# Performance work log

Measured on AMD Instinct MI355X. Metric: run time of the kernel, lower is better.

The kernel has to match this reference:

```python
import jax, jax.numpy as jnp
import numpy as np

N = 4096
F_IN = 256
F_OUT = 64
H = 4
ALPHA = 0.2  # leaky_relu negative slope
NEG_BIG = -9e15


def setup_inputs() -> dict:
    key = jax.random.key(0)
    k1, k2, k3, k4 = jax.random.split(key, 4)
    x = jax.random.normal(k1, (N, F_IN), dtype=jnp.float32)
    adj = jax.random.randint(k2, (N, N), 0, 2, dtype=jnp.int32)
    # xavier-uniform-like init for params
    limW = float(np.sqrt(6.0 / (F_IN + F_OUT)))
    W = jax.random.uniform(k3, (H, F_IN, F_OUT), jnp.float32, -limW, limW)
    lima = float(np.sqrt(6.0 / (2 * F_OUT + 1)))
    a = jax.random.uniform(k4, (H, 2 * F_OUT, 1), jnp.float32, -lima, lima)
    return {"x": x, "adj": adj, "W": W, "a": a}


def reference(x, adj, W, a):
    # Wh[h,n,o] = x @ W[h]
    Wh = jnp.einsum('nf,hfo->hno', x, W)
    # split attention vector: e[h,i,j] = leaky_relu(a1.Wh_i + a2.Wh_j)
    a1 = a[:, :F_OUT, 0]   # [H, F_OUT]
    a2 = a[:, F_OUT:, 0]   # [H, F_OUT]
    s1 = jnp.einsum('hno,ho->hn', Wh, a1)  # [H, N]
    s2 = jnp.einsum('hno,ho->hn', Wh, a2)  # [H, N]
    e = jax.nn.leaky_relu(s1[:, :, None] + s2[:, None, :], ALPHA)  # [H, N, N]
    e = jnp.where(adj[None, :, :] > 0, e, NEG_BIG)
    att = jax.nn.softmax(e, axis=-1)
    # dropout=0 (eval-mode reference)
    h_prime = jnp.einsum('hij,hjo->hio', att, Wh)  # [H, N, F_OUT]
    # concat heads -> [N, H*F_OUT]
    return jnp.transpose(h_prime, (1, 0, 2)).reshape(N, H * F_OUT)
```

## Files before the change

kernel.cpp:

```cpp
#include <hip/hip_runtime.h>

#define NN 4096
#define FIN 256
#define FOUT 64
#define NH 4

using f32x4 = __attribute__((ext_vector_type(4))) float;
using s16x8 = __attribute__((ext_vector_type(8))) short;
typedef unsigned long long u64;

__device__ __forceinline__ unsigned short f32_to_bf16_rne(float f) {
    unsigned b = __float_as_uint(f);
    b += 0x7FFFu + ((b >> 16) & 1u);
    return (unsigned short)(b >> 16);
}

__global__ __launch_bounds__(256) void k_prep(
    const float* __restrict__ x, const float* __restrict__ W,
    const float* __restrict__ a, const int* __restrict__ adj,
    short* __restrict__ WhT, float* __restrict__ s1, float* __restrict__ s2,
    float* __restrict__ blockmax, u64* __restrict__ packed)
{
    __shared__ unsigned short xs[64 * 256];
    __shared__ unsigned short wt[64 * 256];
    __shared__ float s2red[16];
    const int bx = blockIdx.x;
    const int t = threadIdx.x;

    if (bx >= 256) {
        const int lane = t & 63;
        const int jc = t >> 6;
        const int row = bx - 256;
        const int g = lane >> 4;
        const int li = lane & 15;
        const int* ap = adj + (size_t)row * NN + jc * 1024 + lane * 4;
        int4 v0 = *(const int4*)(ap);
        int4 v1 = *(const int4*)(ap + 256);
        int4 v2 = *(const int4*)(ap + 512);
        int4 v3 = *(const int4*)(ap + 768);
        u64 words[4];
        int4 vv[4] = {v0, v1, v2, v3};
        #pragma unroll
        for (int k = 0; k < 4; ++k) {
            unsigned b = (vv[k].x != 0 ? 1u : 0u) | (vv[k].y != 0 ? 2u : 0u)
                       | (vv[k].z != 0 ? 4u : 0u) | (vv[k].w != 0 ? 8u : 0u);
            u64 field = (u64)b << (4 * li);
            field |= __shfl_xor(field, 1, 64);
            field |= __shfl_xor(field, 2, 64);
            field |= __shfl_xor(field, 4, 64);
            field |= __shfl_xor(field, 8, 64);
            words[k] = field;
        }
        if (li == 0) {
            #pragma unroll
            for (int k = 0; k < 4; ++k)
                packed[(size_t)(jc * 16 + 4 * k + g) * NN + row] = words[k];
        }
        return;
    }

    const int nb = bx & 63, h = bx >> 6;
    const int n0 = nb * 64;
    {
        const float4* xg = reinterpret_cast<const float4*>(x + (size_t)n0 * FIN);
        for (int k = t; k < 64 * FIN / 4; k += 256) {
            float4 v = xg[k];
            int row = k >> 6, fq = k & 63;
            u64 pk = (u64)f32_to_bf16_rne(v.x) | ((u64)f32_to_bf16_rne(v.y) << 16)
                   | ((u64)f32_to_bf16_rne(v.z) << 32) | ((u64)f32_to_bf16_rne(v.w) << 48);
            int byte = (row * 512 + fq * 8) ^ ((row & 7) << 4);
            *(u64*)((char*)xs + byte) = pk;
        }
        const float* Wg = W + (size_t)h * FIN * FOUT;
        for (int k = t; k < FIN * FOUT; k += 256) {
            int f = k >> 6, o = k & 63;
            unsigned short wv = f32_to_bf16_rne(Wg[k]);
            int byte = (o * 512 + f * 2) ^ ((o & 7) << 4);
            *(unsigned short*)((char*)wt + byte) = wv;
        }
    }
    __syncthreads();
    const int lane = t & 63, wv_ = t >> 6;
    const int rowA = lane & 15;
    const int kq = (lane >> 4) * 8;
    const int i0 = wv_ * 16;
    f32x4 acc[4];
    #pragma unroll
    for (int c = 0; c < 4; ++c) acc[c] = (f32x4){0.f, 0.f, 0.f, 0.f};
    const int arow = i0 + rowA;
    #pragma unroll
    for (int kb = 0; kb < FIN; kb += 32) {
        int ab = (arow * 512 + (kb + kq) * 2) ^ ((arow & 7) << 4);
        s16x8 af = *(const s16x8*)((char*)xs + ab);
        #pragma unroll
        for (int c = 0; c < 4; ++c) {
            int col = c * 16 + rowA;
            int bb = (col * 512 + (kb + kq) * 2) ^ ((col & 7) << 4);
            s16x8 bf = *(const s16x8*)((char*)wt + bb);
            acc[c] = __builtin_amdgcn_mfma_f32_16x16x32_bf16(af, bf, acc[c], 0, 0, 0);
        }
    }
    const int q0 = (lane >> 4) * 4;
    const float L2E = 1.4426950408889634f;
    float v1acc[4] = {0.f, 0.f, 0.f, 0.f}, v2acc[4] = {0.f, 0.f, 0.f, 0.f};
    #pragma unroll
    for (int c = 0; c < 4; ++c) {
        int col = c * 16 + rowA;
        float a1v = a[h * (2 * FOUT) + col];
        float a2v = a[h * (2 * FOUT) + FOUT + col];
        short* wp = WhT + ((size_t)(h * FOUT + col)) * NN + n0 + i0 + q0;
        alignas(8) unsigned short tmp[4];
        #pragma unroll
        for (int q = 0; q < 4; ++q) {
            float v = acc[c][q];
            tmp[q] = f32_to_bf16_rne(v);
            v1acc[q] = fmaf(v, a1v, v1acc[q]);
            v2acc[q] = fmaf(v, a2v, v2acc[q]);
        }
        __builtin_memcpy(wp, tmp, 8);
    }
    float wmax = -3.0e38f;
    #pragma unroll
    for (int q = 0; q < 4; ++q) {
        float v1 = v1acc[q] * L2E, v2 = v2acc[q] * L2E;
        #pragma unroll
        for (int d = 1; d < 16; d <<= 1) {
            v1 += __shfl_xor(v1, d, 64);
            v2 += __shfl_xor(v2, d, 64);
        }
        if (rowA == 0) {
            int n = n0 + i0 + q0 + q;
            s1[h * NN + n] = v1;
            s2[h * NN + n] = v2;
            wmax = fmaxf(wmax, v2);
        }
    }
    if (rowA == 0) s2red[wv_ * 4 + (lane >> 4)] = wmax;
    __syncthreads();
    if (t == 0) {
        float m = s2red[0];
        #pragma unroll
        for (int i = 1; i < 16; ++i) m = fmaxf(m, s2red[i]);
        blockmax[h * 64 + nb] = m;
    }
}

__global__ __launch_bounds__(1024, 4) void k_attn(
    const u64* __restrict__ packed, const short* __restrict__ WhT,
    const float* __restrict__ s1, const float* __restrict__ blockmax,
    const float* __restrict__ s2, float* __restrict__ out)
{
    __shared__ __align__(16) char smraw[16 * 1040 * 4];
    const int t = threadIdx.x;
    const int lane = t & 63;
    const int wid = t >> 6;
    const int rg = wid >> 2;
    const int jq = wid & 3;
    const int ib64 = blockIdx.x;
    const int h = blockIdx.y;
    const int row16 = lane & 15;
    const int kbase = (lane >> 4) * 8;
    const int irow = ib64 * 64 + rg * 16 + row16;

    float bm = blockmax[h * 64 + lane];
    #pragma unroll
    for (int d = 32; d >= 1; d >>= 1) bm = fmaxf(bm, __shfl_xor(bm, d, 64));
    const float s1v = s1[h * NN + irow];
    const float ttv = s1v + bm;
    const float M = fmaxf(ttv, 0.2f * ttv);
    const float c1v = s1v - M;
    const float c2v = fmaf(0.2f, s1v, -M);

    f32x4 acc[4], acc_l;
    #pragma unroll
    for (int c = 0; c < 4; ++c) acc[c] = (f32x4){0.f, 0.f, 0.f, 0.f};
    acc_l = (f32x4){0.f, 0.f, 0.f, 0.f};
    s16x8 ones;
    #pragma unroll
    for (int i = 0; i < 8; ++i) ones[i] = (short)0x3F80;

    const float* s2q = s2 + h * NN + kbase;
    const u64*   mb  = packed + irow;

    const int gt = rg * 64 + lane;
    const int so = gt >> 3;
    const int sj = (gt & 7) * 8;
    const short* wsrc = WhT + (size_t)h * FOUT * NN;
    char* btb = smraw + jq * 16384;
    const int wb0 = (so * 128 + sj * 2) ^ ((so & 7) << 4);
    const int wb1 = ((so + 32) * 128 + sj * 2) ^ ((so & 7) << 4);

    int rd[4][2];
    #pragma unroll
    for (int c = 0; c < 4; ++c) {
        int o = c * 16 + row16;
        #pragma unroll
        for (int hf = 0; hf < 2; ++hf)
            rd[c][hf] = (o * 128 + (hf * 32 + kbase) * 2) ^ ((o & 7) << 4);
    }

    auto mk = [&](float sa, float sb, unsigned bits, int q0) -> unsigned {
        float e0 = fmaxf(c1v + sa, fmaf(0.2f, sa, c2v));
        float e1 = fmaxf(c1v + sb, fmaf(0.2f, sb, c2v));
        float p0 = __builtin_amdgcn_exp2f(e0);
        float p1 = __builtin_amdgcn_exp2f(e1);
        p0 = (bits & (1u << q0)) ? p0 : 0.f;
        p1 = (bits & (2u << q0)) ? p1 : 0.f;
        unsigned pk;
        asm("v_cvt_pk_bf16_f32 %0, %1, %2" : "=v"(pk) : "v"(p0), "v"(p1));
        return pk;
    };

    const int jbase = jq * 1024;
    auto body = [&](int jb, char* btr, char* btw, u64 cm, f32x4 (&cs)[4],
                    u64& nm, f32x4 (&ns)[4]) {
        int jn = jb + 64;
        int jpf = (jn < jbase + 1024) ? jn : jbase;
        s16x8 st0 = *(const s16x8*)(wsrc + (size_t)so * NN + jpf + sj);
        s16x8 st1 = *(const s16x8*)(wsrc + (size_t)(so + 32) * NN + jpf + sj);
        nm = mb[(size_t)(jpf >> 6) * NN];
        ns[0] = *(const f32x4*)(s2q + jpf);
        ns[1] = *(const f32x4*)(s2q + jpf + 4);
        ns[2] = *(const f32x4*)(s2q + jpf + 32);
        ns[3] = *(const f32x4*)(s2q + jpf + 36);
        unsigned ml8 = ((unsigned)cm >> kbase) & 0xFFu;
        unsigned mh8 = ((unsigned)(cm >> 32) >> kbase) & 0xFFu;
        s16x8 A0, A1;
        unsigned* A0u = reinterpret_cast<unsigned*>(&A0);
        unsigned* A1u = reinterpret_cast<unsigned*>(&A1);
        A0u[0] = mk(cs[0][0], cs[0][1], ml8, 0);
        A0u[1] = mk(cs[0][2], cs[0][3], ml8, 2);
        A0u[2] = mk(cs[1][0], cs[1][1], ml8, 4);
        A0u[3] = mk(cs[1][2], cs[1][3], ml8, 6);
        A1u[0] = mk(cs[2][0], cs[2][1], mh8, 0);
        A1u[1] = mk(cs[2][2], cs[2][3], mh8, 2);
        A1u[2] = mk(cs[3][0], cs[3][1], mh8, 4);
        A1u[3] = mk(cs[3][2], cs[3][3], mh8, 6);
        *(s16x8*)(btw + wb0) = st0;
        *(s16x8*)(btw + wb1) = st1;
        s16x8 b00 = *(const s16x8*)(btr + rd[0][0]);
        s16x8 b01 = *(const s16x8*)(btr + rd[0][1]);
        s16x8 b10 = *(const s16x8*)(btr + rd[1][0]);
        s16x8 b11 = *(const s16x8*)(btr + rd[1][1]);
        s16x8 b20 = *(const s16x8*)(btr + rd[2][0]);
        s16x8 b21 = *(const s16x8*)(btr + rd[2][1]);
        s16x8 b30 = *(const s16x8*)(btr + rd[3][0]);
        s16x8 b31 = *(const s16x8*)(btr + rd[3][1]);
        acc_l  = __builtin_amdgcn_mfma_f32_16x16x32_bf16(A0, ones, acc_l, 0, 0, 0);
        acc_l  = __builtin_amdgcn_mfma_f32_16x16x32_bf16(A1, ones, acc_l, 0, 0, 0);
        acc[0] = __builtin_amdgcn_mfma_f32_16x16x32_bf16(A0, b00, acc[0], 0, 0, 0);
        acc[0] = __builtin_amdgcn_mfma_f32_16x16x32_bf16(A1, b01, acc[0], 0, 0, 0);
        acc[1] = __builtin_amdgcn_mfma_f32_16x16x32_bf16(A0, b10, acc[1], 0, 0, 0);
        acc[1] = __builtin_amdgcn_mfma_f32_16x16x32_bf16(A1, b11, acc[1], 0, 0, 0);
        acc[2] = __builtin_amdgcn_mfma_f32_16x16x32_bf16(A0, b20, acc[2], 0, 0, 0);
        acc[2] = __builtin_amdgcn_mfma_f32_16x16x32_bf16(A1, b21, acc[2], 0, 0, 0);
        acc[3] = __builtin_amdgcn_mfma_f32_16x16x32_bf16(A0, b30, acc[3], 0, 0, 0);
        acc[3] = __builtin_amdgcn_mfma_f32_16x16x32_bf16(A1, b31, acc[3], 0, 0, 0);
    };

    u64 m0, m1;
    f32x4 sv0[4], sv1[4];
    int jb = jbase;
    {
        s16x8 st0 = *(const s16x8*)(wsrc + (size_t)so * NN + jb + sj);
        s16x8 st1 = *(const s16x8*)(wsrc + (size_t)(so + 32) * NN + jb + sj);
        *(s16x8*)(btb + wb0) = st0;
        *(s16x8*)(btb + wb1) = st1;
        m0 = mb[(size_t)(jb >> 6) * NN];
        sv0[0] = *(const f32x4*)(s2q + jb);
        sv0[1] = *(const f32x4*)(s2q + jb + 4);
        sv0[2] = *(const f32x4*)(s2q + jb + 32);
        sv0[3] = *(const f32x4*)(s2q + jb + 36);
    }
    __syncthreads();
    #pragma unroll 1
    for (int it = 0; it < 8; ++it) {
        body(jb, btb, btb + 8192, m0, sv0, m1, sv1);
        __syncthreads();
        body(jb + 64, btb + 8192, btb, m1, sv1, m0, sv0);
        __syncthreads();
        jb += 128;
    }

    float* mw = (float*)smraw + wid * 1040;
    #pragma unroll
    for (int c = 0; c < 4; ++c) {
        #pragma unroll
        for (int q = 0; q < 4; ++q) {
            int r = (lane >> 4) * 4 + q;
            int o = c * 16 + row16;
            mw[r * 64 + o] = acc[c][q];
        }
    }
    if (row16 == 0) {
        #pragma unroll
        for (int q = 0; q < 4; ++q) mw[1024 + (lane >> 4) * 4 + q] = acc_l[q];
    }
    __syncthreads();
    if (jq == 0) {
        const float* p0 = (float*)smraw + (rg * 4 + 0) * 1040;
        const float* p1 = (float*)smraw + (rg * 4 + 1) * 1040;
        const float* p2 = (float*)smraw + (rg * 4 + 2) * 1040;
        const float* p3 = (float*)smraw + (rg * 4 + 3) * 1040;
        #pragma unroll
        for (int k = 0; k < 16; ++k) {
            int idx = k * 64 + lane;
            int r = idx >> 6;
            float v = p0[idx] + p1[idx] + p2[idx] + p3[idx];
            float l = p0[1024 + r] + p1[1024 + r] + p2[1024 + r] + p3[1024 + r];
            int n = ib64 * 64 + rg * 16 + r;
            out[(size_t)n * (NH * FOUT) + h * FOUT + (idx & 63)] = v / l;
        }
    }
}

extern "C" void kernel_launch(void* const* d_in, const int* in_sizes, int n_in,
                              void* d_out, int out_size, void* d_ws, size_t ws_size,
                              hipStream_t stream) {
    (void)in_sizes; (void)n_in; (void)out_size; (void)ws_size;
    const float* x  = (const float*)d_in[0];
    const int*  adj = (const int*)d_in[1];
    const float* W  = (const float*)d_in[2];
    const float* a  = (const float*)d_in[3];
    float* out = (float*)d_out;
    char* ws = (char*)d_ws;

    size_t off = 0;
    short* WhT      = (short*)(ws + off); off += (size_t)NH * FOUT * NN * 2;
    float* s1       = (float*)(ws + off); off += (size_t)NH * NN * 4;
    float* s2       = (float*)(ws + off); off += (size_t)NH * NN * 4;
    float* blockmax = (float*)(ws + off); off += (size_t)NH * 64 * 4;
    u64* packed     = (u64*)(ws + off); off += (size_t)(NN / 64) * NN * 8;

    k_prep<<<4352, 256, 0, stream>>>(x, W, a, adj, WhT, s1, s2, blockmax, packed);
    k_attn<<<dim3(64, NH), 1024, 0, stream>>>(packed, WhT, s1, blockmax, s2, out);
}
```

Baseline: 52.95 us.

## Split attention key range across two blocks and merge partials in new kernel

The attention kernel grid gains a z dimension of 2, and each block now covers half of the key columns, so there are 512 blocks instead of 256 on the device. Each block writes its unnormalized partial accumulators and row sums to a workspace buffer. A new merge kernel adds the two partials and divides by the summed normalizer. The aim is better CU occupancy (256 blocks underfill the MI355X), at the cost of an extra launch and a partial-buffer round trip through global memory.

```diff
diff --git a/kernel.cpp b/kernel.cpp
--- a/kernel.cpp
+++ b/kernel.cpp
@@ -148,7 +148,7 @@
 __global__ __launch_bounds__(1024, 4) void k_attn(
     const u64* __restrict__ packed, const short* __restrict__ WhT,
     const float* __restrict__ s1, const float* __restrict__ blockmax,
-    const float* __restrict__ s2, float* __restrict__ out)
+    const float* __restrict__ s2, float* __restrict__ pacc)
 {
     __shared__ __align__(16) char smraw[16 * 1040 * 4];
     const int t = threadIdx.x;
@@ -158,6 +158,7 @@
     const int jq = wid & 3;
     const int ib64 = blockIdx.x;
     const int h = blockIdx.y;
+    const int s = blockIdx.z;
     const int row16 = lane & 15;
     const int kbase = (lane >> 4) * 8;
     const int irow = ib64 * 64 + rg * 16 + row16;
@@ -211,11 +212,11 @@
         return pk;
     };
 
-    const int jbase = jq * 1024;
+    const int jbase = s * 2048 + jq * 512;
     auto body = [&](int jb, char* btr, char* btw, u64 cm, f32x4 (&cs)[4],
                     u64& nm, f32x4 (&ns)[4]) {
         int jn = jb + 64;
-        int jpf = (jn < jbase + 1024) ? jn : jbase;
+        int jpf = (jn < jbase + 512) ? jn : jbase;
         s16x8 st0 = *(const s16x8*)(wsrc + (size_t)so * NN + jpf + sj);
         s16x8 st1 = *(const s16x8*)(wsrc + (size_t)(so + 32) * NN + jpf + sj);
         nm = mb[(size_t)(jpf >> 6) * NN];
@@ -274,7 +275,7 @@
     }
     __syncthreads();
     #pragma unroll 1
-    for (int it = 0; it < 8; ++it) {
+    for (int it = 0; it < 4; ++it) {
         body(jb, btb, btb + 8192, m0, sv0, m1, sv1);
         __syncthreads();
         body(jb + 64, btb + 8192, btb, m1, sv1, m0, sv0);
@@ -302,16 +303,33 @@
         const float* p1 = (float*)smraw + (rg * 4 + 1) * 1040;
         const float* p2 = (float*)smraw + (rg * 4 + 2) * 1040;
         const float* p3 = (float*)smraw + (rg * 4 + 3) * 1040;
+        float* pb = pacc + ((size_t)((ib64 * NH + h) * 2 + s)) * 4160;
         #pragma unroll
         for (int k = 0; k < 16; ++k) {
             int idx = k * 64 + lane;
-            int r = idx >> 6;
             float v = p0[idx] + p1[idx] + p2[idx] + p3[idx];
-            float l = p0[1024 + r] + p1[1024 + r] + p2[1024 + r] + p3[1024 + r];
-            int n = ib64 * 64 + rg * 16 + r;
-            out[(size_t)n * (NH * FOUT) + h * FOUT + (idx & 63)] = v / l;
-        }
-    }
+            pb[(rg * 16 + k) * 64 + lane] = v;
+            if (lane == 0) {
+                float l = p0[1024 + k] + p1[1024 + k] + p2[1024 + k] + p3[1024 + k];
+                pb[4096 + rg * 16 + k] = l;
+            }
+        }
+    }
+}
+
+__global__ __launch_bounds__(256) void k_merge(const float* __restrict__ pacc,
+                                               float* __restrict__ out)
+{
+    const int idx = blockIdx.x * 256 + threadIdx.x;
+    const int o = idx & 63;
+    const int h = (idx >> 6) & 3;
+    const int n = idx >> 8;
+    const int ib = n >> 6, r = n & 63;
+    const float* b0 = pacc + ((size_t)((ib * NH + h) * 2 + 0)) * 4160;
+    const float* b1 = pacc + ((size_t)((ib * NH + h) * 2 + 1)) * 4160;
+    float v = b0[r * 64 + o] + b1[r * 64 + o];
+    float l = b0[4096 + r] + b1[4096 + r];
+    out[idx] = v / l;
 }
 
 extern "C" void kernel_launch(void* const* d_in, const int* in_sizes, int n_in,
@@ -331,7 +349,9 @@
     float* s2       = (float*)(ws + off); off += (size_t)NH * NN * 4;
     float* blockmax = (float*)(ws + off); off += (size_t)NH * 64 * 4;
     u64* packed     = (u64*)(ws + off); off += (size_t)(NN / 64) * NN * 8;
+    float* pacc     = (float*)(ws + off); off += (size_t)64 * NH * 2 * 4160 * 4;
 
     k_prep<<<4352, 256, 0, stream>>>(x, W, a, adj, WhT, s1, s2, blockmax, packed);
-    k_attn<<<dim3(64, NH), 1024, 0, stream>>>(packed, WhT, s1, blockmax, s2, out);
-}
+    k_attn<<<dim3(64, NH, 2), 1024, 0, stream>>>(packed, WhT, s1, blockmax, s2, pacc);
+    k_merge<<<NN * NH * FOUT / 256, 256, 0, stream>>>(pacc, out);
+}
```

Measured after the change: 62.61 us. 18.3% more time.
